# Kernel tuning notes

Hardware: AMD Instinct MI355X
Metric: run time of the kernel (lower is better)

Reference implementation:

```python
import jax, jax.numpy as jnp
import numpy as np

H = 8          # num_heads
DK = 128       # head_k_dim = 2048*0.5/8
DV = 256       # head_v_dim = 2048*1.0/8
CHUNK = 64     # chunk length of chunk_gla
GLN = 16.0     # gate_logit_normalizer
EPS = 1e-5     # norm_eps


def setup_inputs() -> dict:
    key = jax.random.key(0)
    k1, k2, k3, k4, k5 = jax.random.split(key, 5)
    B, T, D = 4, 2048, 2048
    Kdim, Vdim, R = 1024, 2048, 16
    return {
        "segment": jax.random.normal(k1, (B, T, D), jnp.float32),
        "norm_w": jnp.ones((D,), jnp.float32),
        "Wk": jax.random.normal(k2, (D, Kdim), jnp.float32) * 0.02,
        "Wv": jax.random.normal(k3, (D, Vdim), jnp.float32) * 0.02,
        "Wg1": jax.random.normal(k4, (D, R), jnp.float32) * 0.02,
        "Wg2": jax.random.normal(k5, (R, Kdim), jnp.float32) * 0.02,
        "bg2": jnp.zeros((Kdim,), jnp.float32),
        "initial_state": jnp.zeros((B, H, DK, DV), jnp.float32),
    }


def _gla_final_state(segment, norm_w, Wk, Wv, Wg1, Wg2, bg2, initial_state):
    B, T, D = segment.shape
    # RMSNorm
    x = segment * jax.lax.rsqrt(jnp.mean(segment * segment, axis=-1, keepdims=True) + EPS)
    x = x * norm_w
    # projections (q_proj does not affect the returned state; omitted)
    k = (x @ Wk).reshape(B, T, H, DK)
    v = (x @ Wv).reshape(B, T, H, DV)
    gk = jax.nn.log_sigmoid((x @ Wg1) @ Wg2 + bg2).reshape(B, T, H, DK) / GLN

    NC = T // CHUNK
    # [NC, B, H, C, d] time-chunked, chunk-major for scan
    kc = k.reshape(B, NC, CHUNK, H, DK).transpose(1, 0, 3, 2, 4)
    vc = v.reshape(B, NC, CHUNK, H, DV).transpose(1, 0, 3, 2, 4)
    gc = gk.reshape(B, NC, CHUNK, H, DK).transpose(1, 0, 3, 2, 4)

    b = jnp.cumsum(gc, axis=3)                       # inclusive intra-chunk log-decay
    b_last = b[..., -1:, :]                          # [NC,B,H,1,DK]
    decay_k = jnp.exp(b_last - b)                    # decay from step t to chunk end
    chunk_decay = jnp.exp(b[..., -1, :])             # [NC,B,H,DK] decay of carried state
    # per-chunk outer-product accumulation: sum_t (k_t * decay) v_t^T
    kv = jnp.einsum('nbhck,nbhcv->nbhkv', kc * decay_k, vc)

    def step(S, inp):
        d, u = inp
        return S * d[..., None] + u, None

    S, _ = jax.lax.scan(step, initial_state, (chunk_decay, kv))
    return S


def reference(segment, norm_w, Wk, Wv, Wg1, Wg2, bg2, initial_state):
    return _gla_final_state(segment, norm_w, Wk, Wv, Wg1, Wg2, bg2, initial_state)
```

## Files before the change

kernel.cpp:

```cpp
#include <hip/hip_runtime.h>
#include <math.h>

#define Hh 8
#define DKc 128
#define DVc 256
#define CHUNKc 64
#define GLNf 16.0f
#define EPSf 1e-5f

#define Bb 4
#define Tt 2048
#define Dd 2048
#define KDIM 1024
#define VDIM 2048
#define Mrows 8192
#define NCHUNK 32
#define NBH 32

typedef short bf16x8 __attribute__((ext_vector_type(8)));
typedef float f32x4 __attribute__((ext_vector_type(4)));
typedef ushort ushort8v __attribute__((ext_vector_type(8)));

__device__ inline ushort f2bf(float f) {
  unsigned u = __float_as_uint(f);
  unsigned r = (u + 0x7fffu + ((u >> 16) & 1u)) >> 16;
  return (ushort)r;
}
__device__ inline float bf2f(ushort u) {
  return __uint_as_float(((unsigned)u) << 16);
}
__device__ inline float logsig(float g) {
  return fminf(g, 0.f) - __logf(1.f + __expf(-fabsf(g)));
}

__global__ __launch_bounds__(256) void rmsnorm_kernel(const float* __restrict__ seg,
                                                      const float* __restrict__ norm_w,
                                                      ushort* __restrict__ xb) {
  int row = blockIdx.x;
  int t = threadIdx.x;
  const float4* p = (const float4*)(seg + (size_t)row * Dd);
  float4 a = p[t];
  float4 b = p[t + 256];
  float ss = a.x * a.x + a.y * a.y + a.z * a.z + a.w * a.w +
             b.x * b.x + b.y * b.y + b.z * b.z + b.w * b.w;
#pragma unroll
  for (int off = 32; off > 0; off >>= 1) ss += __shfl_down(ss, off);
  __shared__ float red[4];
  if ((t & 63) == 0) red[t >> 6] = ss;
  __syncthreads();
  float tot = red[0] + red[1] + red[2] + red[3];
  float scale = rsqrtf(tot * (1.0f / (float)Dd) + EPSf);
  const float4* w4 = (const float4*)norm_w;
  float4 wa = w4[t], wb = w4[t + 256];
  ushort4 oa, ob;
  oa.x = f2bf(a.x * scale * wa.x);
  oa.y = f2bf(a.y * scale * wa.y);
  oa.z = f2bf(a.z * scale * wa.z);
  oa.w = f2bf(a.w * scale * wa.w);
  ob.x = f2bf(b.x * scale * wb.x);
  ob.y = f2bf(b.y * scale * wb.y);
  ob.z = f2bf(b.z * scale * wb.z);
  ob.w = f2bf(b.w * scale * wb.w);
  ushort4* o4 = (ushort4*)(xb + (size_t)row * Dd);
  o4[t] = oa;
  o4[t + 256] = ob;
}

__global__ __launch_bounds__(256) void transpose_cast_kernel(const float* __restrict__ in,
                                                             ushort* __restrict__ out,
                                                             int N, int Nstride, int nbase) {
  const int K = 2048;
  __shared__ float tile[32][33];
  int k0 = blockIdx.x * 32;
  int nloc0 = blockIdx.y * 32;
  int tx = threadIdx.x & 31;
  int ty = threadIdx.x >> 5;
#pragma unroll
  for (int i = 0; i < 32; i += 8) {
    int k = k0 + ty + i;
    int n = nbase + nloc0 + tx;
    float v = (n < N) ? in[(size_t)k * Nstride + n] : 0.0f;
    tile[ty + i][tx] = v;
  }
  __syncthreads();
#pragma unroll
  for (int i = 0; i < 32; i += 8) {
    int nloc = nloc0 + ty + i;
    int k = k0 + tx;
    out[(size_t)nloc * K + k] = f2bf(tile[tx][ty + i]);
  }
}

__global__ __launch_bounds__(256) void transpose_all_kernel(const float* __restrict__ Wv,
                                                            const float* __restrict__ Wk,
                                                            const float* __restrict__ Wg1,
                                                            ushort* __restrict__ Wall) {
  const int K = 2048;
  __shared__ float tile[32][33];
  int k0 = blockIdx.x * 32;
  int n0 = blockIdx.y * 32;
  const float* src;
  int N, stride, nb;
  if (n0 < 2048) {
    src = Wv; N = 2048; stride = 2048; nb = n0;
  } else if (n0 < 3072) {
    src = Wk; N = 1024; stride = 1024; nb = n0 - 2048;
  } else {
    src = Wg1; N = 16; stride = 16; nb = n0 - 3072;
  }
  int tx = threadIdx.x & 31;
  int ty = threadIdx.x >> 5;
#pragma unroll
  for (int i = 0; i < 32; i += 8) {
    int k = k0 + ty + i;
    int n = nb + tx;
    tile[ty + i][tx] = (n < N) ? src[(size_t)k * stride + n] : 0.0f;
  }
  __syncthreads();
#pragma unroll
  for (int i = 0; i < 32; i += 8) {
    Wall[(size_t)(n0 + ty + i) * K + k0 + tx] = f2bf(tile[tx][ty + i]);
  }
}

template <int MODE>
__global__ __launch_bounds__(256) void gemm_kernel(const ushort* __restrict__ A,
                                                   const ushort* __restrict__ Bt,
                                                   void* __restrict__ Cv,
                                                   int N, int K, int bnOff) {
  __shared__ __align__(16) ushort As[128 * 32];
  __shared__ __align__(16) ushort Bs[128 * 32];
  int bm = blockIdx.x;
  int bn = blockIdx.y + bnOff;
  int wave = threadIdx.x >> 6;
  int lane = threadIdx.x & 63;
  int wm = wave >> 1, wn = wave & 1;
  int lrow = lane & 15;
  int quad = lane >> 4;
  int rowInChunk = lane >> 2;
  int kElem = (lane & 3) * 8;

  f32x4 acc[4][4] = {};
  const size_t Kz = (size_t)K;

  for (int kk = 0; kk < K; kk += 32) {
#pragma unroll
    for (int r = 0; r < 2; ++r) {
      int chunk = wave * 2 + r;
      int arow = chunk * 16 + rowInChunk;
      const ushort* ga = A + ((size_t)(bm * 128 + arow)) * Kz + kk + kElem;
      const ushort* gb = Bt + ((size_t)(blockIdx.y * 128 + arow)) * Kz + kk + kElem;
      __builtin_amdgcn_global_load_lds((__attribute__((address_space(1))) void*)ga,
                                       (__attribute__((address_space(3))) void*)(As + chunk * 512),
                                       16, 0, 0);
      __builtin_amdgcn_global_load_lds((__attribute__((address_space(1))) void*)gb,
                                       (__attribute__((address_space(3))) void*)(Bs + chunk * 512),
                                       16, 0, 0);
    }
    __syncthreads();
    bf16x8 af[4], bfr[4];
#pragma unroll
    for (int i = 0; i < 4; ++i) {
      int r = wm * 64 + i * 16 + lrow;
      af[i] = *(const bf16x8*)(As + r * 32 + quad * 8);
    }
#pragma unroll
    for (int j = 0; j < 4; ++j) {
      int r = wn * 64 + j * 16 + lrow;
      bfr[j] = *(const bf16x8*)(Bs + r * 32 + quad * 8);
    }
#pragma unroll
    for (int i = 0; i < 4; ++i)
#pragma unroll
      for (int j = 0; j < 4; ++j)
        acc[i][j] = __builtin_amdgcn_mfma_f32_16x16x32_bf16(af[i], bfr[j], acc[i][j], 0, 0, 0);
    __syncthreads();
  }

#pragma unroll
  for (int i = 0; i < 4; ++i) {
    int m0 = bm * 128 + wm * 64 + i * 16 + quad * 4;
#pragma unroll
    for (int j = 0; j < 4; ++j) {
      int col = bn * 128 + wn * 64 + j * 16 + lrow;
      if (MODE == 0) {
#pragma unroll
        for (int rg = 0; rg < 4; ++rg)
          ((float*)Cv)[(size_t)(m0 + rg) * N + col] = acc[i][j][rg];
      } else if (MODE == 1) {
#pragma unroll
        for (int rg = 0; rg < 4; ++rg)
          ((ushort*)Cv)[(size_t)(m0 + rg) * N + col] = f2bf(acc[i][j][rg]);
      } else {
        int b = m0 >> 11, tloc = m0 & 2047;
        int h = col >> 8, vv = col & 255;
        ushort4 o;
        o.x = f2bf(acc[i][j][0]);
        o.y = f2bf(acc[i][j][1]);
        o.z = f2bf(acc[i][j][2]);
        o.w = f2bf(acc[i][j][3]);
        *(ushort4*)((ushort*)Cv + ((size_t)((b * 8 + h) * 256 + vv)) * 2048 + tloc) = o;
      }
    }
  }
}

__global__ __launch_bounds__(256) void gemm_fused_kernel(const ushort* __restrict__ A,
                                                         const ushort* __restrict__ Wall,
                                                         ushort* __restrict__ vT,
                                                         ushort* __restrict__ kT,
                                                         float* __restrict__ g1) {
  __shared__ __align__(16) ushort As[128 * 32];
  __shared__ __align__(16) ushort Bs[128 * 32];
  int bm = blockIdx.x;
  int bn = blockIdx.y;
  int wave = threadIdx.x >> 6;
  int lane = threadIdx.x & 63;
  int wm = wave >> 1, wn = wave & 1;
  int lrow = lane & 15;
  int quad = lane >> 4;
  int rowInChunk = lane >> 2;
  int kElem = (lane & 3) * 8;

  f32x4 acc[4][4] = {};
  for (int kk = 0; kk < Dd; kk += 32) {
#pragma unroll
    for (int r = 0; r < 2; ++r) {
      int chunk = wave * 2 + r;
      int arow = chunk * 16 + rowInChunk;
      const ushort* ga = A + ((size_t)(bm * 128 + arow)) * Dd + kk + kElem;
      const ushort* gb = Wall + ((size_t)(bn * 128 + arow)) * Dd + kk + kElem;
      __builtin_amdgcn_global_load_lds((__attribute__((address_space(1))) void*)ga,
                                       (__attribute__((address_space(3))) void*)(As + chunk * 512),
                                       16, 0, 0);
      __builtin_amdgcn_global_load_lds((__attribute__((address_space(1))) void*)gb,
                                       (__attribute__((address_space(3))) void*)(Bs + chunk * 512),
                                       16, 0, 0);
    }
    __syncthreads();
    bf16x8 af[4], bfr[4];
#pragma unroll
    for (int i = 0; i < 4; ++i) af[i] = *(const bf16x8*)(As + (wm * 64 + i * 16 + lrow) * 32 + quad * 8);
#pragma unroll
    for (int j = 0; j < 4; ++j) bfr[j] = *(const bf16x8*)(Bs + (wn * 64 + j * 16 + lrow) * 32 + quad * 8);
#pragma unroll
    for (int i = 0; i < 4; ++i)
#pragma unroll
      for (int j = 0; j < 4; ++j)
        acc[i][j] = __builtin_amdgcn_mfma_f32_16x16x32_bf16(af[i], bfr[j], acc[i][j], 0, 0, 0);
    __syncthreads();
  }

#pragma unroll
  for (int i = 0; i < 4; ++i) {
    int m0 = bm * 128 + wm * 64 + i * 16 + quad * 4;
    int b = m0 >> 11, tloc = m0 & 2047;
#pragma unroll
    for (int j = 0; j < 4; ++j) {
      int col = bn * 128 + wn * 64 + j * 16 + lrow;
      if (bn < 16) {
        int h = col >> 8, vv = col & 255;
        ushort4 o;
        o.x = f2bf(acc[i][j][0]);
        o.y = f2bf(acc[i][j][1]);
        o.z = f2bf(acc[i][j][2]);
        o.w = f2bf(acc[i][j][3]);
        *(ushort4*)(vT + ((size_t)((b * 8 + h) * 256 + vv)) * 2048 + tloc) = o;
      } else if (bn < 24) {
        int ck = col - 2048;
        int h = ck >> 7, kd = ck & 127;
        ushort4 o;
        o.x = f2bf(acc[i][j][0]);
        o.y = f2bf(acc[i][j][1]);
        o.z = f2bf(acc[i][j][2]);
        o.w = f2bf(acc[i][j][3]);
        *(ushort4*)(kT + ((size_t)((b * 8 + h) * 128 + kd)) * 2048 + tloc) = o;
      } else {
        int cg = col - 3072;
#pragma unroll
        for (int rg = 0; rg < 4; ++rg)
          g1[(size_t)(m0 + rg) * 128 + cg] = acc[i][j][rg];
      }
    }
  }
}

__global__ __launch_bounds__(128) void chunksum_kernel(const float* __restrict__ g1,
                                                       const float* __restrict__ Wg2,
                                                       const float* __restrict__ bg2,
                                                       float* __restrict__ L) {
  int n = blockIdx.x, bh = blockIdx.y;
  int b = bh >> 3, h = bh & 7;
  int t = threadIdx.x;
  int kdg = h * DKc + t;
  int trow = b * Tt + n * CHUNKc;
  __shared__ float g1s[CHUNKc * 16];
#pragma unroll
  for (int i = 0; i < 8; ++i) {
    int flat = i * 128 + t;
    int c = flat >> 4, r = flat & 15;
    g1s[flat] = g1[(size_t)(trow + c) * 128 + r];
  }
  float wc[16];
#pragma unroll
  for (int r = 0; r < 16; ++r) wc[r] = Wg2[r * KDIM + kdg];
  float bias = bg2[kdg];
  __syncthreads();
  float sum = 0.f;
  for (int c = 0; c < CHUNKc; ++c) {
    float dot = bias;
#pragma unroll
    for (int r = 0; r < 16; ++r) dot = fmaf(g1s[c * 16 + r], wc[r], dot);
    sum += logsig(dot) * (1.0f / GLNf);
  }
  L[((size_t)bh * NCHUNK + n) * DKc + t] = sum;
}

template <int KLAY>
__global__ __launch_bounds__(128) void weight_kernel(const float* __restrict__ g1,
                                                     const float* __restrict__ Wg2,
                                                     const float* __restrict__ bg2,
                                                     const ushort* __restrict__ kb,
                                                     const float* __restrict__ L,
                                                     ushort* __restrict__ kwT,
                                                     float* __restrict__ eBtot) {
  int n = blockIdx.x, bh = blockIdx.y;
  int b = bh >> 3, h = bh & 7;
  int t = threadIdx.x;
  int kdg = h * DKc + t;
  int trow = b * Tt + n * CHUNKc;
  __shared__ float g1s[CHUNKc * 16];
#pragma unroll
  for (int i = 0; i < 8; ++i) {
    int flat = i * 128 + t;
    int c = flat >> 4, r = flat & 15;
    g1s[flat] = g1[(size_t)(trow + c) * 128 + r];
  }
  float wc[16];
#pragma unroll
  for (int r = 0; r < 16; ++r) wc[r] = Wg2[r * KDIM + kdg];
  float bias = bg2[kdg];

  float suffix = 0.f, Ln = 0.f, Btot = 0.f;
#pragma unroll
  for (int m = 0; m < NCHUNK; ++m) {
    float Lm = L[((size_t)bh * NCHUNK + m) * DKc + t];
    if (m > n) suffix += Lm;
    if (m == n) Ln = Lm;
    Btot += Lm;
  }
  if (n == 0) eBtot[bh * DKc + t] = __expf(Btot);
  __syncthreads();

  float run = 0.f;
  size_t obase = ((size_t)bh * DKc + t) * (size_t)Tt + (size_t)n * CHUNKc;
  for (int cg = 0; cg < 8; ++cg) {
    ushort8v kw8, k8;
    if (KLAY == 1) k8 = *(const ushort8v*)(kwT + obase + cg * 8);
#pragma unroll
    for (int j = 0; j < 8; ++j) {
      int c = cg * 8 + j;
      float dot = bias;
#pragma unroll
      for (int r = 0; r < 16; ++r) dot = fmaf(g1s[c * 16 + r], wc[r], dot);
      run += logsig(dot) * (1.0f / GLNf);
      float w = __expf(suffix + Ln - run);
      float kv = (KLAY == 1) ? bf2f(k8[j]) : bf2f(kb[(size_t)(trow + c) * KDIM + kdg]);
      kw8[j] = f2bf(kv * w);
    }
    *(ushort8v*)(kwT + obase + cg * 8) = kw8;
  }
}

__global__ __launch_bounds__(256) void kv_gemm_kernel(const ushort* __restrict__ kwT,
                                                      const ushort* __restrict__ vT,
                                                      float* __restrict__ Spart) {
  __shared__ __align__(16) ushort As[128 * 32];
  __shared__ __align__(16) ushort Bs[128 * 32];
  int bn = blockIdx.x;
  int bh = blockIdx.y;
  int ks = blockIdx.z;
  const ushort* A = kwT + (size_t)bh * DKc * Tt;
  const ushort* B = vT + (size_t)(bh * DVc + bn * 128) * Tt;
  int wave = threadIdx.x >> 6;
  int lane = threadIdx.x & 63;
  int wm = wave >> 1, wn = wave & 1;
  int lrow = lane & 15;
  int quad = lane >> 4;
  int rowInChunk = lane >> 2;
  int kElem = (lane & 3) * 8;

  f32x4 acc[4][4] = {};
  int kk0 = ks * 512;
  for (int kk = kk0; kk < kk0 + 512; kk += 32) {
#pragma unroll
    for (int r = 0; r < 2; ++r) {
      int chunk = wave * 2 + r;
      int arow = chunk * 16 + rowInChunk;
      const ushort* ga = A + (size_t)arow * Tt + kk + kElem;
      const ushort* gb = B + (size_t)arow * Tt + kk + kElem;
      __builtin_amdgcn_global_load_lds((__attribute__((address_space(1))) void*)ga,
                                       (__attribute__((address_space(3))) void*)(As + chunk * 512),
                                       16, 0, 0);
      __builtin_amdgcn_global_load_lds((__attribute__((address_space(1))) void*)gb,
                                       (__attribute__((address_space(3))) void*)(Bs + chunk * 512),
                                       16, 0, 0);
    }
    __syncthreads();
    bf16x8 af[4], bfr[4];
#pragma unroll
    for (int i = 0; i < 4; ++i) af[i] = *(const bf16x8*)(As + (wm * 64 + i * 16 + lrow) * 32 + quad * 8);
#pragma unroll
    for (int j = 0; j < 4; ++j) bfr[j] = *(const bf16x8*)(Bs + (wn * 64 + j * 16 + lrow) * 32 + quad * 8);
#pragma unroll
    for (int i = 0; i < 4; ++i)
#pragma unroll
      for (int j = 0; j < 4; ++j)
        acc[i][j] = __builtin_amdgcn_mfma_f32_16x16x32_bf16(af[i], bfr[j], acc[i][j], 0, 0, 0);
    __syncthreads();
  }

  float* Sp = Spart + ((size_t)ks * NBH + bh) * (DKc * DVc);
#pragma unroll
  for (int i = 0; i < 4; ++i) {
    int row0 = wm * 64 + i * 16 + quad * 4;
#pragma unroll
    for (int j = 0; j < 4; ++j) {
      int col = bn * 128 + wn * 64 + j * 16 + lrow;
#pragma unroll
      for (int rg = 0; rg < 4; ++rg)
        Sp[(size_t)(row0 + rg) * DVc + col] = acc[i][j][rg];
    }
  }
}

__global__ __launch_bounds__(256) void reduce_kernel(const float* __restrict__ Spart,
                                                     const float* __restrict__ eBtot,
                                                     const float* __restrict__ S0,
                                                     float* __restrict__ out) {
  int i4 = blockIdx.x * 256 + threadIdx.x;
  int idx = i4 * 4;
  int bh = idx >> 15;
  int kd = (idx >> 8) & 127;
  float e = eBtot[bh * DKc + kd];
  float4 a = ((const float4*)S0)[i4];
  float4 p0 = ((const float4*)Spart)[i4];
  float4 p1 = ((const float4*)Spart)[i4 + 262144];
  float4 p2 = ((const float4*)Spart)[i4 + 524288];
  float4 p3 = ((const float4*)Spart)[i4 + 786432];
  float4 r;
  r.x = a.x * e + p0.x + p1.x + p2.x + p3.x;
  r.y = a.y * e + p0.y + p1.y + p2.y + p3.y;
  r.z = a.z * e + p0.z + p1.z + p2.z + p3.z;
  r.w = a.w * e + p0.w + p1.w + p2.w + p3.w;
  ((float4*)out)[i4] = r;
}

extern "C" void kernel_launch(void* const* d_in, const int* in_sizes, int n_in,
                              void* d_out, int out_size, void* d_ws, size_t ws_size,
                              hipStream_t stream) {
  const float* seg = (const float*)d_in[0];
  const float* norm_w = (const float*)d_in[1];
  const float* Wk = (const float*)d_in[2];
  const float* Wv = (const float*)d_in[3];
  const float* Wg1 = (const float*)d_in[4];
  const float* Wg2 = (const float*)d_in[5];
  const float* bg2 = (const float*)d_in[6];
  const float* S0 = (const float*)d_in[7];
  float* out = (float*)d_out;
  char* ws = (char*)d_ws;

  const size_t FUSED_NEED = 83886080ULL + 13107200ULL + 524288ULL + 16384ULL;

  if (ws_size >= FUSED_NEED) {
    char* regA = ws;
    char* regB = ws + (size_t)32 * 1024 * 1024;
    char* regD = ws + (size_t)64 * 1024 * 1024;
    char* regC = ws + (size_t)80 * 1024 * 1024;
    float* Lbuf = (float*)(regC + 13107200);
    float* eBtot = (float*)(regC + 13107200 + 524288);

    ushort* xb = (ushort*)regA;
    float* Spart = (float*)regA;
    ushort* vT = (ushort*)regB;
    ushort* kwT = (ushort*)regD;
    ushort* Wall = (ushort*)regC;
    float* g1buf = (float*)d_out;

    rmsnorm_kernel<<<Mrows, 256, 0, stream>>>(seg, norm_w, xb);
    transpose_all_kernel<<<dim3(64, 100), 256, 0, stream>>>(Wv, Wk, Wg1, Wall);
    gemm_fused_kernel<<<dim3(64, 25), 256, 0, stream>>>(xb, Wall, vT, kwT, g1buf);
    chunksum_kernel<<<dim3(NCHUNK, NBH), 128, 0, stream>>>(g1buf, Wg2, bg2, Lbuf);
    weight_kernel<1><<<dim3(NCHUNK, NBH), 128, 0, stream>>>(g1buf, Wg2, bg2, kwT, Lbuf, kwT, eBtot);
    kv_gemm_kernel<<<dim3(2, NBH, 4), 256, 0, stream>>>(kwT, vT, Spart);
    reduce_kernel<<<1024, 256, 0, stream>>>(Spart, eBtot, S0, out);
  } else {
    char* regA = ws;
    char* regB = ws + (size_t)32 * 1024 * 1024;
    char* regD = ws + (size_t)64 * 1024 * 1024;
    char* regC = ws + (size_t)80 * 1024 * 1024;
    float* eBtot = (float*)(ws + (size_t)84 * 1024 * 1024);

    ushort* xb = (ushort*)regA;
    ushort* kwT = (ushort*)regA;
    float* Spart = (float*)(regA + 16777216);
    ushort* vT = (ushort*)regB;
    ushort* kb = (ushort*)regD;
    ushort* WvTh = (ushort*)regC;
    ushort* WkT = (ushort*)regC;
    float* g1buf = (float*)regC;
    ushort* WgT = (ushort*)d_out;
    float* Lbuf = (float*)((char*)d_out + 2097152);

    rmsnorm_kernel<<<Mrows, 256, 0, stream>>>(seg, norm_w, xb);

    transpose_cast_kernel<<<dim3(64, 32), 256, 0, stream>>>(Wv, WvTh, VDIM, VDIM, 0);
    gemm_kernel<2><<<dim3(64, 8), 256, 0, stream>>>(xb, WvTh, vT, VDIM, Dd, 0);
    transpose_cast_kernel<<<dim3(64, 32), 256, 0, stream>>>(Wv, WvTh, VDIM, VDIM, 1024);
    gemm_kernel<2><<<dim3(64, 8), 256, 0, stream>>>(xb, WvTh, vT, VDIM, Dd, 8);

    transpose_cast_kernel<<<dim3(64, 32), 256, 0, stream>>>(Wk, WkT, KDIM, KDIM, 0);
    gemm_kernel<1><<<dim3(64, 8), 256, 0, stream>>>(xb, WkT, kb, KDIM, Dd, 0);

    transpose_cast_kernel<<<dim3(64, 4), 256, 0, stream>>>(Wg1, WgT, 16, 16, 0);
    gemm_kernel<0><<<dim3(64, 1), 256, 0, stream>>>(xb, WgT, g1buf, 128, Dd, 0);

    chunksum_kernel<<<dim3(NCHUNK, NBH), 128, 0, stream>>>(g1buf, Wg2, bg2, Lbuf);
    weight_kernel<0><<<dim3(NCHUNK, NBH), 128, 0, stream>>>(g1buf, Wg2, bg2, kb, Lbuf, kwT, eBtot);
    kv_gemm_kernel<<<dim3(2, NBH, 4), 256, 0, stream>>>(kwT, vT, Spart);
    reduce_kernel<<<1024, 256, 0, stream>>>(Spart, eBtot, S0, out);
  }
}
```

Before: 376.2 us.

## Reassociate KV state as (kw^T x) Wv to skip the V projection

Stops materializing v = x@Wv. Each head's state is now computed as (kw^T x) followed by a multiply with that head's slice of Wv, which cuts total matmul FLOPs roughly by the size of the V projection. It adds a transpose of the normalized input, a bf16 intermediate Y per (batch, head), and a final GEMM that fuses the S0 decay term, replacing the split-K kv GEMM and its reduce kernel. The risks are extra bf16 rounding on Y, the extra transpose traffic, and a final GEMM that launches only 64 blocks. The low-workspace fallback path is removed.

```diff
diff --git a/kernel.cpp b/kernel.cpp
--- a/kernel.cpp
+++ b/kernel.cpp
@@ -66,31 +66,6 @@
   o4[t + 256] = ob;
 }
 
-__global__ __launch_bounds__(256) void transpose_cast_kernel(const float* __restrict__ in,
-                                                             ushort* __restrict__ out,
-                                                             int N, int Nstride, int nbase) {
-  const int K = 2048;
-  __shared__ float tile[32][33];
-  int k0 = blockIdx.x * 32;
-  int nloc0 = blockIdx.y * 32;
-  int tx = threadIdx.x & 31;
-  int ty = threadIdx.x >> 5;
-#pragma unroll
-  for (int i = 0; i < 32; i += 8) {
-    int k = k0 + ty + i;
-    int n = nbase + nloc0 + tx;
-    float v = (n < N) ? in[(size_t)k * Nstride + n] : 0.0f;
-    tile[ty + i][tx] = v;
-  }
-  __syncthreads();
-#pragma unroll
-  for (int i = 0; i < 32; i += 8) {
-    int nloc = nloc0 + ty + i;
-    int k = k0 + tx;
-    out[(size_t)nloc * K + k] = f2bf(tile[tx][ty + i]);
-  }
-}
-
 __global__ __launch_bounds__(256) void transpose_all_kernel(const float* __restrict__ Wv,
                                                             const float* __restrict__ Wk,
                                                             const float* __restrict__ Wg1,
@@ -123,93 +98,27 @@
   }
 }
 
-template <int MODE>
-__global__ __launch_bounds__(256) void gemm_kernel(const ushort* __restrict__ A,
-                                                   const ushort* __restrict__ Bt,
-                                                   void* __restrict__ Cv,
-                                                   int N, int K, int bnOff) {
-  __shared__ __align__(16) ushort As[128 * 32];
-  __shared__ __align__(16) ushort Bs[128 * 32];
-  int bm = blockIdx.x;
-  int bn = blockIdx.y + bnOff;
-  int wave = threadIdx.x >> 6;
-  int lane = threadIdx.x & 63;
-  int wm = wave >> 1, wn = wave & 1;
-  int lrow = lane & 15;
-  int quad = lane >> 4;
-  int rowInChunk = lane >> 2;
-  int kElem = (lane & 3) * 8;
-
-  f32x4 acc[4][4] = {};
-  const size_t Kz = (size_t)K;
-
-  for (int kk = 0; kk < K; kk += 32) {
-#pragma unroll
-    for (int r = 0; r < 2; ++r) {
-      int chunk = wave * 2 + r;
-      int arow = chunk * 16 + rowInChunk;
-      const ushort* ga = A + ((size_t)(bm * 128 + arow)) * Kz + kk + kElem;
-      const ushort* gb = Bt + ((size_t)(blockIdx.y * 128 + arow)) * Kz + kk + kElem;
-      __builtin_amdgcn_global_load_lds((__attribute__((address_space(1))) void*)ga,
-                                       (__attribute__((address_space(3))) void*)(As + chunk * 512),
-                                       16, 0, 0);
-      __builtin_amdgcn_global_load_lds((__attribute__((address_space(1))) void*)gb,
-                                       (__attribute__((address_space(3))) void*)(Bs + chunk * 512),
-                                       16, 0, 0);
-    }
-    __syncthreads();
-    bf16x8 af[4], bfr[4];
-#pragma unroll
-    for (int i = 0; i < 4; ++i) {
-      int r = wm * 64 + i * 16 + lrow;
-      af[i] = *(const bf16x8*)(As + r * 32 + quad * 8);
-    }
-#pragma unroll
-    for (int j = 0; j < 4; ++j) {
-      int r = wn * 64 + j * 16 + lrow;
-      bfr[j] = *(const bf16x8*)(Bs + r * 32 + quad * 8);
-    }
-#pragma unroll
-    for (int i = 0; i < 4; ++i)
-#pragma unroll
-      for (int j = 0; j < 4; ++j)
-        acc[i][j] = __builtin_amdgcn_mfma_f32_16x16x32_bf16(af[i], bfr[j], acc[i][j], 0, 0, 0);
-    __syncthreads();
-  }
-
-#pragma unroll
-  for (int i = 0; i < 4; ++i) {
-    int m0 = bm * 128 + wm * 64 + i * 16 + quad * 4;
-#pragma unroll
-    for (int j = 0; j < 4; ++j) {
-      int col = bn * 128 + wn * 64 + j * 16 + lrow;
-      if (MODE == 0) {
-#pragma unroll
-        for (int rg = 0; rg < 4; ++rg)
-          ((float*)Cv)[(size_t)(m0 + rg) * N + col] = acc[i][j][rg];
-      } else if (MODE == 1) {
-#pragma unroll
-        for (int rg = 0; rg < 4; ++rg)
-          ((ushort*)Cv)[(size_t)(m0 + rg) * N + col] = f2bf(acc[i][j][rg]);
-      } else {
-        int b = m0 >> 11, tloc = m0 & 2047;
-        int h = col >> 8, vv = col & 255;
-        ushort4 o;
-        o.x = f2bf(acc[i][j][0]);
-        o.y = f2bf(acc[i][j][1]);
-        o.z = f2bf(acc[i][j][2]);
-        o.w = f2bf(acc[i][j][3]);
-        *(ushort4*)((ushort*)Cv + ((size_t)((b * 8 + h) * 256 + vv)) * 2048 + tloc) = o;
-      }
-    }
-  }
-}
-
-__global__ __launch_bounds__(256) void gemm_fused_kernel(const ushort* __restrict__ A,
-                                                         const ushort* __restrict__ Wall,
-                                                         ushort* __restrict__ vT,
-                                                         ushort* __restrict__ kT,
-                                                         float* __restrict__ g1) {
+__global__ __launch_bounds__(256) void transpose_x_kernel(const ushort* __restrict__ xb,
+                                                          ushort* __restrict__ xT) {
+  __shared__ ushort tile[32][34];
+  int b = blockIdx.z;
+  int t0 = blockIdx.x * 32;
+  int d0 = blockIdx.y * 32;
+  int tx = threadIdx.x & 31;
+  int ty = threadIdx.x >> 5;
+#pragma unroll
+  for (int i = 0; i < 32; i += 8)
+    tile[ty + i][tx] = xb[((size_t)b * Tt + t0 + ty + i) * Dd + d0 + tx];
+  __syncthreads();
+#pragma unroll
+  for (int i = 0; i < 32; i += 8)
+    xT[((size_t)b * Dd + d0 + ty + i) * Tt + t0 + tx] = tile[tx][ty + i];
+}
+
+__global__ __launch_bounds__(256) void gemm_kg_kernel(const ushort* __restrict__ A,
+                                                      const ushort* __restrict__ Wallk,
+                                                      ushort* __restrict__ kT,
+                                                      float* __restrict__ g1) {
   __shared__ __align__(16) ushort As[128 * 32];
   __shared__ __align__(16) ushort Bs[128 * 32];
   int bm = blockIdx.x;
@@ -229,7 +138,7 @@
       int chunk = wave * 2 + r;
       int arow = chunk * 16 + rowInChunk;
       const ushort* ga = A + ((size_t)(bm * 128 + arow)) * Dd + kk + kElem;
-      const ushort* gb = Wall + ((size_t)(bn * 128 + arow)) * Dd + kk + kElem;
+      const ushort* gb = Wallk + ((size_t)(bn * 128 + arow)) * Dd + kk + kElem;
       __builtin_amdgcn_global_load_lds((__attribute__((address_space(1))) void*)ga,
                                        (__attribute__((address_space(3))) void*)(As + chunk * 512),
                                        16, 0, 0);
@@ -258,17 +167,8 @@
 #pragma unroll
     for (int j = 0; j < 4; ++j) {
       int col = bn * 128 + wn * 64 + j * 16 + lrow;
-      if (bn < 16) {
-        int h = col >> 8, vv = col & 255;
-        ushort4 o;
-        o.x = f2bf(acc[i][j][0]);
-        o.y = f2bf(acc[i][j][1]);
-        o.z = f2bf(acc[i][j][2]);
-        o.w = f2bf(acc[i][j][3]);
-        *(ushort4*)(vT + ((size_t)((b * 8 + h) * 256 + vv)) * 2048 + tloc) = o;
-      } else if (bn < 24) {
-        int ck = col - 2048;
-        int h = ck >> 7, kd = ck & 127;
+      if (bn < 8) {
+        int h = col >> 7, kd = col & 127;
         ushort4 o;
         o.x = f2bf(acc[i][j][0]);
         o.y = f2bf(acc[i][j][1]);
@@ -276,10 +176,136 @@
         o.w = f2bf(acc[i][j][3]);
         *(ushort4*)(kT + ((size_t)((b * 8 + h) * 128 + kd)) * 2048 + tloc) = o;
       } else {
-        int cg = col - 3072;
+        int cg = col - 1024;
 #pragma unroll
         for (int rg = 0; rg < 4; ++rg)
           g1[(size_t)(m0 + rg) * 128 + cg] = acc[i][j][rg];
+      }
+    }
+  }
+}
+
+__global__ __launch_bounds__(256) void gemm_y_kernel(const ushort* __restrict__ kwT,
+                                                     const ushort* __restrict__ xT,
+                                                     ushort* __restrict__ Y) {
+  __shared__ __align__(16) ushort As[128 * 32];
+  __shared__ __align__(16) ushort Bs[128 * 32];
+  int bn = blockIdx.x;
+  int bh = blockIdx.y;
+  int b = bh >> 3;
+  const ushort* A = kwT + (size_t)bh * DKc * Tt;
+  const ushort* B = xT + (size_t)b * Dd * Tt;
+  int wave = threadIdx.x >> 6;
+  int lane = threadIdx.x & 63;
+  int wm = wave >> 1, wn = wave & 1;
+  int lrow = lane & 15;
+  int quad = lane >> 4;
+  int rowInChunk = lane >> 2;
+  int kElem = (lane & 3) * 8;
+
+  f32x4 acc[4][4] = {};
+  for (int kk = 0; kk < Tt; kk += 32) {
+#pragma unroll
+    for (int r = 0; r < 2; ++r) {
+      int chunk = wave * 2 + r;
+      int arow = chunk * 16 + rowInChunk;
+      const ushort* ga = A + (size_t)arow * Tt + kk + kElem;
+      const ushort* gb = B + ((size_t)(bn * 128 + arow)) * Tt + kk + kElem;
+      __builtin_amdgcn_global_load_lds((__attribute__((address_space(1))) void*)ga,
+                                       (__attribute__((address_space(3))) void*)(As + chunk * 512),
+                                       16, 0, 0);
+      __builtin_amdgcn_global_load_lds((__attribute__((address_space(1))) void*)gb,
+                                       (__attribute__((address_space(3))) void*)(Bs + chunk * 512),
+                                       16, 0, 0);
+    }
+    __syncthreads();
+    bf16x8 af[4], bfr[4];
+#pragma unroll
+    for (int i = 0; i < 4; ++i) af[i] = *(const bf16x8*)(As + (wm * 64 + i * 16 + lrow) * 32 + quad * 8);
+#pragma unroll
+    for (int j = 0; j < 4; ++j) bfr[j] = *(const bf16x8*)(Bs + (wn * 64 + j * 16 + lrow) * 32 + quad * 8);
+#pragma unroll
+    for (int i = 0; i < 4; ++i)
+#pragma unroll
+      for (int j = 0; j < 4; ++j)
+        acc[i][j] = __builtin_amdgcn_mfma_f32_16x16x32_bf16(af[i], bfr[j], acc[i][j], 0, 0, 0);
+    __syncthreads();
+  }
+
+#pragma unroll
+  for (int i = 0; i < 4; ++i) {
+    int row0 = wm * 64 + i * 16 + quad * 4;
+#pragma unroll
+    for (int j = 0; j < 4; ++j) {
+      int col = bn * 128 + wn * 64 + j * 16 + lrow;
+#pragma unroll
+      for (int rg = 0; rg < 4; ++rg)
+        Y[((size_t)bh * DKc + row0 + rg) * Dd + col] = f2bf(acc[i][j][rg]);
+    }
+  }
+}
+
+__global__ __launch_bounds__(256) void gemm_out_kernel(const ushort* __restrict__ Y,
+                                                       const ushort* __restrict__ WvT,
+                                                       const float* __restrict__ eBtot,
+                                                       const float* __restrict__ S0,
+                                                       float* __restrict__ out) {
+  __shared__ __align__(16) ushort As[128 * 32];
+  __shared__ __align__(16) ushort Bs[128 * 32];
+  int bn = blockIdx.x;
+  int bh = blockIdx.y;
+  int h = bh & 7;
+  const ushort* A = Y + (size_t)bh * DKc * Dd;
+  const ushort* B = WvT + (size_t)(h * DVc + bn * 128) * Dd;
+  int wave = threadIdx.x >> 6;
+  int lane = threadIdx.x & 63;
+  int wm = wave >> 1, wn = wave & 1;
+  int lrow = lane & 15;
+  int quad = lane >> 4;
+  int rowInChunk = lane >> 2;
+  int kElem = (lane & 3) * 8;
+
+  f32x4 acc[4][4] = {};
+  for (int kk = 0; kk < Dd; kk += 32) {
+#pragma unroll
+    for (int r = 0; r < 2; ++r) {
+      int chunk = wave * 2 + r;
+      int arow = chunk * 16 + rowInChunk;
+      const ushort* ga = A + (size_t)arow * Dd + kk + kElem;
+      const ushort* gb = B + (size_t)arow * Dd + kk + kElem;
+      __builtin_amdgcn_global_load_lds((__attribute__((address_space(1))) void*)ga,
+                                       (__attribute__((address_space(3))) void*)(As + chunk * 512),
+                                       16, 0, 0);
+      __builtin_amdgcn_global_load_lds((__attribute__((address_space(1))) void*)gb,
+                                       (__attribute__((address_space(3))) void*)(Bs + chunk * 512),
+                                       16, 0, 0);
+    }
+    __syncthreads();
+    bf16x8 af[4], bfr[4];
+#pragma unroll
+    for (int i = 0; i < 4; ++i) af[i] = *(const bf16x8*)(As + (wm * 64 + i * 16 + lrow) * 32 + quad * 8);
+#pragma unroll
+    for (int j = 0; j < 4; ++j) bfr[j] = *(const bf16x8*)(Bs + (wn * 64 + j * 16 + lrow) * 32 + quad * 8);
+#pragma unroll
+    for (int i = 0; i < 4; ++i)
+#pragma unroll
+      for (int j = 0; j < 4; ++j)
+        acc[i][j] = __builtin_amdgcn_mfma_f32_16x16x32_bf16(af[i], bfr[j], acc[i][j], 0, 0, 0);
+    __syncthreads();
+  }
+
+  size_t base = (size_t)bh * DKc * DVc;
+#pragma unroll
+  for (int i = 0; i < 4; ++i) {
+    int row0 = wm * 64 + i * 16 + quad * 4;
+#pragma unroll
+    for (int j = 0; j < 4; ++j) {
+      int col = bn * 128 + wn * 64 + j * 16 + lrow;
+#pragma unroll
+      for (int rg = 0; rg < 4; ++rg) {
+        int r = row0 + rg;
+        out[base + (size_t)r * DVc + col] =
+            S0[base + (size_t)r * DVc + col] * eBtot[bh * DKc + r] + acc[i][j][rg];
       }
     }
   }
@@ -316,11 +342,9 @@
   L[((size_t)bh * NCHUNK + n) * DKc + t] = sum;
 }
 
-template <int KLAY>
 __global__ __launch_bounds__(128) void weight_kernel(const float* __restrict__ g1,
                                                      const float* __restrict__ Wg2,
                                                      const float* __restrict__ bg2,
-                                                     const ushort* __restrict__ kb,
                                                      const float* __restrict__ L,
                                                      ushort* __restrict__ kwT,
                                                      float* __restrict__ eBtot) {
@@ -355,8 +379,8 @@
   float run = 0.f;
   size_t obase = ((size_t)bh * DKc + t) * (size_t)Tt + (size_t)n * CHUNKc;
   for (int cg = 0; cg < 8; ++cg) {
-    ushort8v kw8, k8;
-    if (KLAY == 1) k8 = *(const ushort8v*)(kwT + obase + cg * 8);
+    ushort8v kw8;
+    ushort8v k8 = *(const ushort8v*)(kwT + obase + cg * 8);
 #pragma unroll
     for (int j = 0; j < 8; ++j) {
       int c = cg * 8 + j;
@@ -365,95 +389,10 @@
       for (int r = 0; r < 16; ++r) dot = fmaf(g1s[c * 16 + r], wc[r], dot);
       run += logsig(dot) * (1.0f / GLNf);
       float w = __expf(suffix + Ln - run);
-      float kv = (KLAY == 1) ? bf2f(k8[j]) : bf2f(kb[(size_t)(trow + c) * KDIM + kdg]);
-      kw8[j] = f2bf(kv * w);
+      kw8[j] = f2bf(bf2f(k8[j]) * w);
     }
     *(ushort8v*)(kwT + obase + cg * 8) = kw8;
   }
-}
-
-__global__ __launch_bounds__(256) void kv_gemm_kernel(const ushort* __restrict__ kwT,
-                                                      const ushort* __restrict__ vT,
-                                                      float* __restrict__ Spart) {
-  __shared__ __align__(16) ushort As[128 * 32];
-  __shared__ __align__(16) ushort Bs[128 * 32];
-  int bn = blockIdx.x;
-  int bh = blockIdx.y;
-  int ks = blockIdx.z;
-  const ushort* A = kwT + (size_t)bh * DKc * Tt;
-  const ushort* B = vT + (size_t)(bh * DVc + bn * 128) * Tt;
-  int wave = threadIdx.x >> 6;
-  int lane = threadIdx.x & 63;
-  int wm = wave >> 1, wn = wave & 1;
-  int lrow = lane & 15;
-  int quad = lane >> 4;
-  int rowInChunk = lane >> 2;
-  int kElem = (lane & 3) * 8;
-
-  f32x4 acc[4][4] = {};
-  int kk0 = ks * 512;
-  for (int kk = kk0; kk < kk0 + 512; kk += 32) {
-#pragma unroll
-    for (int r = 0; r < 2; ++r) {
-      int chunk = wave * 2 + r;
-      int arow = chunk * 16 + rowInChunk;
-      const ushort* ga = A + (size_t)arow * Tt + kk + kElem;
-      const ushort* gb = B + (size_t)arow * Tt + kk + kElem;
-      __builtin_amdgcn_global_load_lds((__attribute__((address_space(1))) void*)ga,
-                                       (__attribute__((address_space(3))) void*)(As + chunk * 512),
-                                       16, 0, 0);
-      __builtin_amdgcn_global_load_lds((__attribute__((address_space(1))) void*)gb,
-                                       (__attribute__((address_space(3))) void*)(Bs + chunk * 512),
-                                       16, 0, 0);
-    }
-    __syncthreads();
-    bf16x8 af[4], bfr[4];
-#pragma unroll
-    for (int i = 0; i < 4; ++i) af[i] = *(const bf16x8*)(As + (wm * 64 + i * 16 + lrow) * 32 + quad * 8);
-#pragma unroll
-    for (int j = 0; j < 4; ++j) bfr[j] = *(const bf16x8*)(Bs + (wn * 64 + j * 16 + lrow) * 32 + quad * 8);
-#pragma unroll
-    for (int i = 0; i < 4; ++i)
-#pragma unroll
-      for (int j = 0; j < 4; ++j)
-        acc[i][j] = __builtin_amdgcn_mfma_f32_16x16x32_bf16(af[i], bfr[j], acc[i][j], 0, 0, 0);
-    __syncthreads();
-  }
-
-  float* Sp = Spart + ((size_t)ks * NBH + bh) * (DKc * DVc);
-#pragma unroll
-  for (int i = 0; i < 4; ++i) {
-    int row0 = wm * 64 + i * 16 + quad * 4;
-#pragma unroll
-    for (int j = 0; j < 4; ++j) {
-      int col = bn * 128 + wn * 64 + j * 16 + lrow;
-#pragma unroll
-      for (int rg = 0; rg < 4; ++rg)
-        Sp[(size_t)(row0 + rg) * DVc + col] = acc[i][j][rg];
-    }
-  }
-}
-
-__global__ __launch_bounds__(256) void reduce_kernel(const float* __restrict__ Spart,
-                                                     const float* __restrict__ eBtot,
-                                                     const float* __restrict__ S0,
-                                                     float* __restrict__ out) {
-  int i4 = blockIdx.x * 256 + threadIdx.x;
-  int idx = i4 * 4;
-  int bh = idx >> 15;
-  int kd = (idx >> 8) & 127;
-  float e = eBtot[bh * DKc + kd];
-  float4 a = ((const float4*)S0)[i4];
-  float4 p0 = ((const float4*)Spart)[i4];
-  float4 p1 = ((const float4*)Spart)[i4 + 262144];
-  float4 p2 = ((const float4*)Spart)[i4 + 524288];
-  float4 p3 = ((const float4*)Spart)[i4 + 786432];
-  float4 r;
-  r.x = a.x * e + p0.x + p1.x + p2.x + p3.x;
-  r.y = a.y * e + p0.y + p1.y + p2.y + p3.y;
-  r.z = a.z * e + p0.z + p1.z + p2.z + p3.z;
-  r.w = a.w * e + p0.w + p1.w + p2.w + p3.w;
-  ((float4*)out)[i4] = r;
 }
 
 extern "C" void kernel_launch(void* const* d_in, const int* in_sizes, int n_in,
@@ -470,64 +409,27 @@
   float* out = (float*)d_out;
   char* ws = (char*)d_ws;
 
-  const size_t FUSED_NEED = 83886080ULL + 13107200ULL + 524288ULL + 16384ULL;
-
-  if (ws_size >= FUSED_NEED) {
-    char* regA = ws;
-    char* regB = ws + (size_t)32 * 1024 * 1024;
-    char* regD = ws + (size_t)64 * 1024 * 1024;
-    char* regC = ws + (size_t)80 * 1024 * 1024;
-    float* Lbuf = (float*)(regC + 13107200);
-    float* eBtot = (float*)(regC + 13107200 + 524288);
-
-    ushort* xb = (ushort*)regA;
-    float* Spart = (float*)regA;
-    ushort* vT = (ushort*)regB;
-    ushort* kwT = (ushort*)regD;
-    ushort* Wall = (ushort*)regC;
-    float* g1buf = (float*)d_out;
-
-    rmsnorm_kernel<<<Mrows, 256, 0, stream>>>(seg, norm_w, xb);
-    transpose_all_kernel<<<dim3(64, 100), 256, 0, stream>>>(Wv, Wk, Wg1, Wall);
-    gemm_fused_kernel<<<dim3(64, 25), 256, 0, stream>>>(xb, Wall, vT, kwT, g1buf);
-    chunksum_kernel<<<dim3(NCHUNK, NBH), 128, 0, stream>>>(g1buf, Wg2, bg2, Lbuf);
-    weight_kernel<1><<<dim3(NCHUNK, NBH), 128, 0, stream>>>(g1buf, Wg2, bg2, kwT, Lbuf, kwT, eBtot);
-    kv_gemm_kernel<<<dim3(2, NBH, 4), 256, 0, stream>>>(kwT, vT, Spart);
-    reduce_kernel<<<1024, 256, 0, stream>>>(Spart, eBtot, S0, out);
-  } else {
-    char* regA = ws;
-    char* regB = ws + (size_t)32 * 1024 * 1024;
-    char* regD = ws + (size_t)64 * 1024 * 1024;
-    char* regC = ws + (size_t)80 * 1024 * 1024;
-    float* eBtot = (float*)(ws + (size_t)84 * 1024 * 1024);
-
-    ushort* xb = (ushort*)regA;
-    ushort* kwT = (ushort*)regA;
-    float* Spart = (float*)(regA + 16777216);
-    ushort* vT = (ushort*)regB;
-    ushort* kb = (ushort*)regD;
-    ushort* WvTh = (ushort*)regC;
-    ushort* WkT = (ushort*)regC;
-    float* g1buf = (float*)regC;
-    ushort* WgT = (ushort*)d_out;
-    float* Lbuf = (float*)((char*)d_out + 2097152);
-
-    rmsnorm_kernel<<<Mrows, 256, 0, stream>>>(seg, norm_w, xb);
-
-    transpose_cast_kernel<<<dim3(64, 32), 256, 0, stream>>>(Wv, WvTh, VDIM, VDIM, 0);
-    gemm_kernel<2><<<dim3(64, 8), 256, 0, stream>>>(xb, WvTh, vT, VDIM, Dd, 0);
-    transpose_cast_kernel<<<dim3(64, 32), 256, 0, stream>>>(Wv, WvTh, VDIM, VDIM, 1024);
-    gemm_kernel<2><<<dim3(64, 8), 256, 0, stream>>>(xb, WvTh, vT, VDIM, Dd, 8);
-
-    transpose_cast_kernel<<<dim3(64, 32), 256, 0, stream>>>(Wk, WkT, KDIM, KDIM, 0);
-    gemm_kernel<1><<<dim3(64, 8), 256, 0, stream>>>(xb, WkT, kb, KDIM, Dd, 0);
-
-    transpose_cast_kernel<<<dim3(64, 4), 256, 0, stream>>>(Wg1, WgT, 16, 16, 0);
-    gemm_kernel<0><<<dim3(64, 1), 256, 0, stream>>>(xb, WgT, g1buf, 128, Dd, 0);
-
-    chunksum_kernel<<<dim3(NCHUNK, NBH), 128, 0, stream>>>(g1buf, Wg2, bg2, Lbuf);
-    weight_kernel<0><<<dim3(NCHUNK, NBH), 128, 0, stream>>>(g1buf, Wg2, bg2, kb, Lbuf, kwT, eBtot);
-    kv_gemm_kernel<<<dim3(2, NBH, 4), 256, 0, stream>>>(kwT, vT, Spart);
-    reduce_kernel<<<1024, 256, 0, stream>>>(Spart, eBtot, S0, out);
-  }
-}
+  char* regA = ws;
+  char* regB = ws + (size_t)32 * 1024 * 1024;
+  char* regD = ws + (size_t)64 * 1024 * 1024;
+  char* regC = ws + (size_t)80 * 1024 * 1024;
+  float* Lbuf = (float*)(regC + 13107200);
+  float* eBtot = (float*)(regC + 13107200 + 524288);
+
+  ushort* xb = (ushort*)regA;
+  ushort* Y = (ushort*)regA;
+  ushort* xT = (ushort*)regB;
+  ushort* kwT = (ushort*)regD;
+  ushort* Wall = (ushort*)regC;
+  ushort* Wallk = Wall + (size_t)2048 * 2048;
+  float* g1buf = (float*)d_out;
+
+  rmsnorm_kernel<<<Mrows, 256, 0, stream>>>(seg, norm_w, xb);
+  transpose_all_kernel<<<dim3(64, 100), 256, 0, stream>>>(Wv, Wk, Wg1, Wall);
+  transpose_x_kernel<<<dim3(64, 64, 4), 256, 0, stream>>>(xb, xT);
+  gemm_kg_kernel<<<dim3(64, 9), 256, 0, stream>>>(xb, Wallk, kwT, g1buf);
+  chunksum_kernel<<<dim3(NCHUNK, NBH), 128, 0, stream>>>(g1buf, Wg2, bg2, Lbuf);
+  weight_kernel<<<dim3(NCHUNK, NBH), 128, 0, stream>>>(g1buf, Wg2, bg2, Lbuf, kwT, eBtot);
+  gemm_y_kernel<<<dim3(16, NBH), 256, 0, stream>>>(kwT, xT, Y);
+  gemm_out_kernel<<<dim3(2, NBH), 256, 0, stream>>>(Y, Wall, eBtot, S0, out);
+}
```

New measurement: 360.0 us. -4.3%, faster.
